# Optimization experiments

Measured on AMD Instinct MI355X. Metric: run time of the kernel, lower is better.

Reference implementation:

```python
import jax, jax.numpy as jnp
import numpy as np

B, P, D, H = 2048, 128, 64, 8
DB = 10  # D_obs + D_pos = 7 + 3, hard-coded in the module


def setup_inputs() -> dict:
    key = jax.random.key(0)
    ks = jax.random.split(key, 10)
    s = lambda fan_in: 1.0 / np.sqrt(fan_in)
    return {
        "x": jax.random.normal(ks[0], (B, D), dtype=jnp.float32),
        "b": jax.random.normal(ks[1], (B, P, DB), dtype=jnp.float32),
        "W_kvx": jax.random.uniform(ks[2], (D, 2 * H * D), jnp.float32, -s(D), s(D)),
        "b_kvx": jax.random.uniform(ks[3], (2 * H * D,), jnp.float32, -s(D), s(D)),
        "W_kvb": jax.random.uniform(ks[4], (DB, 2 * H * D), jnp.float32, -s(DB), s(DB)),
        "b_kvb": jax.random.uniform(ks[5], (2 * H * D,), jnp.float32, -s(DB), s(DB)),
        "W_q": jax.random.uniform(ks[6], (D, H * D), jnp.float32, -s(D), s(D)),
        "b_q": jax.random.uniform(ks[7], (H * D,), jnp.float32, -s(D), s(D)),
        "W_f": jax.random.uniform(ks[8], (H * D, D), jnp.float32, -s(H * D), s(H * D)),
        "b_f": jax.random.uniform(ks[9], (D,), jnp.float32, -s(H * D), s(H * D)),
    }


def reference(x, b, W_kvx, b_kvx, W_kvb, b_kvb, W_q, b_q, W_f, b_f):
    Bn, Dx = x.shape
    _, Pn, _ = b.shape
    # dual projections + broadcast add: [B,1,2HD] + [B,P,2HD]
    kv = (x @ W_kvx + b_kvx)[:, None, :] + (jnp.einsum('bpe,ef->bpf', b, W_kvb) + b_kvb)
    k, v = jnp.split(kv, 2, axis=-1)            # each [B,P,H*D]
    k = k.reshape(Bn, Pn, H, Dx)
    v = v.reshape(Bn, Pn, H, Dx)
    q = (x @ W_q + b_q).reshape(Bn, H, Dx)
    dots = jnp.einsum('bphd,bhd->bph', k, q) / np.sqrt(Dx).astype(np.float32)
    # NOTE: faithful to source — softmax over the HEAD axis (last dim of [B,P,H])
    attn = jax.nn.softmax(dots, axis=-1)
    vals = jnp.einsum('bph,bphd->bhd', attn, v)  # sum over positions P
    out = vals.reshape(Bn, H * Dx) @ W_f + b_f
    return out
```

## Files before the change

### kernel.cpp

```cpp
#include <hip/hip_runtime.h>

#define NB   2048
#define NP   128
#define ND   64
#define NH   8
#define NDB  10
#define HD   512
#define F2   1024
#define XQS  1536

__global__ __launch_bounds__(256) void proj_kernel(
    const float* __restrict__ x, const float* __restrict__ W_kvx,
    const float* __restrict__ b_kvx, const float* __restrict__ W_q,
    const float* __restrict__ b_q, float* __restrict__ XQ)
{
    __shared__ float xs[64][68];
    __shared__ float ws_[64][64];
    const int rt = blockIdx.x;
    const int ct = blockIdx.y;
    const int row0 = rt * 64;
    const int t = threadIdx.x;

    #pragma unroll
    for (int it = 0; it < 16; ++it) {
        int i = t + 256 * it;
        int r = i >> 6, k = i & 63;
        xs[k][r] = x[(row0 + r) * ND + k];
    }
    const float* Wsrc; const float* bsrc; int stride, col0;
    if (ct < 16) { Wsrc = W_kvx; bsrc = b_kvx; stride = F2; col0 = ct * 64; }
    else         { Wsrc = W_q;   bsrc = b_q;   stride = HD; col0 = (ct - 16) * 64; }
    #pragma unroll
    for (int it = 0; it < 16; ++it) {
        int i = t + 256 * it;
        int kr = i >> 6, c = i & 63;
        ws_[kr][c] = Wsrc[kr * stride + col0 + c];
    }
    __syncthreads();

    const int tr = t >> 4, tc = t & 15;
    float acc[4][4] = {};
    for (int k = 0; k < 64; ++k) {
        float4 a = *(const float4*)&xs[k][tr * 4];
        float4 w = *(const float4*)&ws_[k][tc * 4];
        float av[4] = {a.x, a.y, a.z, a.w};
        float wv[4] = {w.x, w.y, w.z, w.w};
        #pragma unroll
        for (int i = 0; i < 4; ++i)
            #pragma unroll
            for (int j = 0; j < 4; ++j)
                acc[i][j] = fmaf(av[i], wv[j], acc[i][j]);
    }
    float4 bias = *(const float4*)&bsrc[col0 + tc * 4];
    const int outcol = ct * 64 + tc * 4;
    #pragma unroll
    for (int i = 0; i < 4; ++i) {
        float4 o;
        o.x = acc[i][0] + bias.x;
        o.y = acc[i][1] + bias.y;
        o.z = acc[i][2] + bias.z;
        o.w = acc[i][3] + bias.w;
        *(float4*)&XQ[(row0 + tr * 4 + i) * XQS + outcol] = o;
    }
}

__global__ __launch_bounds__(256) void attn_kernel(
    const float* __restrict__ bmat, const float* __restrict__ W_kvb,
    const float* __restrict__ b_kvb, const float* __restrict__ XQ,
    float* __restrict__ VALS)
{
    __shared__ float q_s[HD];
    __shared__ float bb_s[NP * NDB];
    __shared__ float dot0[NH];
    __shared__ float Wqkb[NDB][NH];
    __shared__ float partA[4][NH];
    __shared__ float partS[4][NDB][NH];
    __shared__ float A_s[NH];
    __shared__ float S_s[NDB][NH];

    const int b = blockIdx.x;
    const int t = threadIdx.x;
    const int lane = t & 63, w = t >> 6;
    const float* xq = XQ + (size_t)b * XQS;

    q_s[t]       = xq[1024 + t];
    q_s[t + 256] = xq[1024 + t + 256];
    #pragma unroll
    for (int it = 0; it < 5; ++it) {
        int i = t + 256 * it;
        bb_s[i] = bmat[(size_t)b * (NP * NDB) + i];
    }
    __syncthreads();

    #pragma unroll
    for (int iter = 0; iter < 2; ++iter) {
        int f = t + iter * 256;
        float prod = (xq[f] + b_kvb[f]) * q_s[f];
        #pragma unroll
        for (int m = 32; m >= 1; m >>= 1) prod += __shfl_xor(prod, m);
        if (lane == 0) dot0[w + iter * 4] = prod;
    }
    {
        int g = t >> 3, l = t & 7;
        #pragma unroll
        for (int ro = 0; ro < 3; ++ro) {
            int o = g + 32 * ro;
            if (o < 80) {
                int e = o >> 3, hh = o & 7;
                float s = 0.f;
                #pragma unroll
                for (int m = 0; m < 8; ++m) {
                    int d = l + m * 8;
                    s += W_kvb[e * F2 + hh * 64 + d] * q_s[hh * 64 + d];
                }
                #pragma unroll
                for (int mm = 1; mm <= 4; mm <<= 1) s += __shfl_xor(s, mm);
                if (l == 0) Wqkb[e][hh] = s;
            }
        }
    }
    __syncthreads();

    const int h = t & 7;
    const int pbase = t >> 3;
    float aA = 0.f;
    float aS[NDB];
    #pragma unroll
    for (int e = 0; e < NDB; ++e) aS[e] = 0.f;
    #pragma unroll
    for (int it = 0; it < 4; ++it) {
        int p = pbase + it * 32;
        float dot = dot0[h];
        #pragma unroll
        for (int e = 0; e < NDB; ++e) dot += bb_s[p * NDB + e] * Wqkb[e][h];
        dot *= 0.125f;
        float m = dot;
        #pragma unroll
        for (int mm = 1; mm <= 4; mm <<= 1) m = fmaxf(m, __shfl_xor(m, mm));
        float ex = __expf(dot - m);
        float s = ex;
        #pragma unroll
        for (int mm = 1; mm <= 4; mm <<= 1) s += __shfl_xor(s, mm);
        float at = ex / s;
        aA += at;
        #pragma unroll
        for (int e = 0; e < NDB; ++e) aS[e] += at * bb_s[p * NDB + e];
    }
    #pragma unroll
    for (int mm = 8; mm <= 32; mm <<= 1) aA += __shfl_xor(aA, mm);
    #pragma unroll
    for (int e = 0; e < NDB; ++e)
        #pragma unroll
        for (int mm = 8; mm <= 32; mm <<= 1) aS[e] += __shfl_xor(aS[e], mm);
    if (lane < 8) {
        partA[w][lane] = aA;
        #pragma unroll
        for (int e = 0; e < NDB; ++e) partS[w][e][lane] = aS[e];
    }
    __syncthreads();
    if (t < 8)  A_s[t] = partA[0][t] + partA[1][t] + partA[2][t] + partA[3][t];
    if (t < 80) {
        int e = t >> 3, hh = t & 7;
        S_s[e][hh] = partS[0][e][hh] + partS[1][e][hh] + partS[2][e][hh] + partS[3][e][hh];
    }
    __syncthreads();

    #pragma unroll
    for (int iter = 0; iter < 2; ++iter) {
        int f = t + iter * 256;
        int hh = f >> 6;
        float val = A_s[hh] * (xq[512 + f] + b_kvb[512 + f]);
        #pragma unroll
        for (int e = 0; e < NDB; ++e) val += S_s[e][hh] * W_kvb[e * F2 + 512 + f];
        VALS[(size_t)b * HD + f] = val;
    }
}

__global__ __launch_bounds__(256) void out_kernel(
    const float* __restrict__ VALS, const float* __restrict__ W_f,
    const float* __restrict__ b_f, float* __restrict__ out)
{
    __shared__ float vs[HD * 10];
    const int t = threadIdx.x;
    const int row0 = blockIdx.x * 8;
    #pragma unroll
    for (int it = 0; it < 16; ++it) {
        int i = t + 256 * it;
        int r = i >> 9, k = i & 511;
        vs[k * 10 + r] = VALS[(size_t)(row0 + r) * HD + k];
    }
    __syncthreads();
    const int j = t & 63, rg = t >> 6;
    float acc0 = 0.f, acc1 = 0.f;
    for (int k = 0; k < 512; ++k) {
        float wv = W_f[k * 64 + j];
        float2 v = *(const float2*)&vs[k * 10 + rg * 2];
        acc0 = fmaf(v.x, wv, acc0);
        acc1 = fmaf(v.y, wv, acc1);
    }
    float bj = b_f[j];
    out[(size_t)(row0 + rg * 2 + 0) * ND + j] = acc0 + bj;
    out[(size_t)(row0 + rg * 2 + 1) * ND + j] = acc1 + bj;
}

extern "C" void kernel_launch(void* const* d_in, const int* in_sizes, int n_in,
                              void* d_out, int out_size, void* d_ws, size_t ws_size,
                              hipStream_t stream)
{
    const float* x     = (const float*)d_in[0];
    const float* bmat  = (const float*)d_in[1];
    const float* W_kvx = (const float*)d_in[2];
    const float* b_kvx = (const float*)d_in[3];
    const float* W_kvb = (const float*)d_in[4];
    const float* b_kvb = (const float*)d_in[5];
    const float* W_q   = (const float*)d_in[6];
    const float* b_q   = (const float*)d_in[7];
    const float* W_f   = (const float*)d_in[8];
    const float* b_f   = (const float*)d_in[9];
    float* out  = (float*)d_out;
    float* XQ   = (float*)d_ws;
    float* VALS = XQ + (size_t)NB * XQS;

    proj_kernel<<<dim3(32, 24), 256, 0, stream>>>(x, W_kvx, b_kvx, W_q, b_q, XQ);
    attn_kernel<<<NB, 256, 0, stream>>>(bmat, W_kvb, b_kvb, XQ, VALS);
    out_kernel<<<NB / 8, 256, 0, stream>>>(VALS, W_f, b_f, out);
}
```

Measured before the change: 125.0 us.

## Fuse projection, attention and output GEMM into one kernel over 4-row batches

Replaces the three-kernel pipeline (projection GEMM, per-row attention, output GEMM) with a single kernel in which each block handles 4 batch rows. Each wave processes one row's attention, and intermediates stay in shared memory instead of going through the global XQ/VALS workspace. This removes two launches and roughly 16 MB of intermediate global traffic. In exchange, each block re-reads the full W_kvx, W_q and W_f weights from global/L2 with only 4-row reuse, and only 512 blocks are launched.

Measured after the change: 105.5 us. -15.6%, faster.

```diff
diff --git a/kernel.cpp b/kernel.cpp
--- a/kernel.cpp
+++ b/kernel.cpp
@@ -1,206 +1,181 @@
 #include <hip/hip_runtime.h>
 
-#define NB   2048
-#define NP   128
-#define ND   64
-#define NH   8
-#define NDB  10
-#define HD   512
-#define F2   1024
-#define XQS  1536
+#define NDB 10
 
-__global__ __launch_bounds__(256) void proj_kernel(
-    const float* __restrict__ x, const float* __restrict__ W_kvx,
-    const float* __restrict__ b_kvx, const float* __restrict__ W_q,
-    const float* __restrict__ b_q, float* __restrict__ XQ)
+__global__ __launch_bounds__(256) void fused_attn(
+    const float* __restrict__ x, const float* __restrict__ bmat,
+    const float* __restrict__ W_kvx, const float* __restrict__ b_kvx,
+    const float* __restrict__ W_kvb, const float* __restrict__ b_kvb,
+    const float* __restrict__ W_q, const float* __restrict__ b_q,
+    const float* __restrict__ W_f, const float* __restrict__ b_f,
+    float* __restrict__ out)
 {
-    __shared__ float xs[64][68];
-    __shared__ float ws_[64][64];
-    const int rt = blockIdx.x;
-    const int ct = blockIdx.y;
-    const int row0 = rt * 64;
+    __shared__ float x_t[64][4];
+    __shared__ float bb_s[4][1280];
+    __shared__ float xp_s[4][1024];
+    __shared__ float q_s[4][512];
+    __shared__ float dot0_s[4][8];
+    __shared__ float Wqkb_s[4][NDB][8];
+    __shared__ float A_s[4][8];
+    __shared__ float S_s[4][NDB][8];
+    __shared__ float vals_s[512][4];
+    __shared__ float pout[4][4][64];
+
     const int t = threadIdx.x;
+    const int b0 = blockIdx.x * 4;
+    const int lane = t & 63;
+    const int w = t >> 6;
 
-    #pragma unroll
-    for (int it = 0; it < 16; ++it) {
-        int i = t + 256 * it;
-        int r = i >> 6, k = i & 63;
-        xs[k][r] = x[(row0 + r) * ND + k];
-    }
-    const float* Wsrc; const float* bsrc; int stride, col0;
-    if (ct < 16) { Wsrc = W_kvx; bsrc = b_kvx; stride = F2; col0 = ct * 64; }
-    else         { Wsrc = W_q;   bsrc = b_q;   stride = HD; col0 = (ct - 16) * 64; }
-    #pragma unroll
-    for (int it = 0; it < 16; ++it) {
-        int i = t + 256 * it;
-        int kr = i >> 6, c = i & 63;
-        ws_[kr][c] = Wsrc[kr * stride + col0 + c];
+    x_t[t & 63][t >> 6] = x[b0 * 64 + t];
+    {
+        const float4* src = (const float4*)(bmat + (size_t)b0 * 1280);
+        float4* dst = (float4*)bb_s;
+        #pragma unroll
+        for (int it = 0; it < 5; ++it) dst[t + 256 * it] = src[t + 256 * it];
     }
     __syncthreads();
 
-    const int tr = t >> 4, tc = t & 15;
-    float acc[4][4] = {};
-    for (int k = 0; k < 64; ++k) {
-        float4 a = *(const float4*)&xs[k][tr * 4];
-        float4 w = *(const float4*)&ws_[k][tc * 4];
-        float av[4] = {a.x, a.y, a.z, a.w};
-        float wv[4] = {w.x, w.y, w.z, w.w};
+    {
+        float accKV[4][4] = {};
+        float accQ[4][2] = {};
+        const float* pkv = W_kvx + t;
+        const float* pq  = W_q  + t;
+        #pragma unroll 4
+        for (int k = 0; k < 64; ++k) {
+            float4 xv = *(const float4*)&x_t[k][0];
+            float xr[4] = {xv.x, xv.y, xv.z, xv.w};
+            float wkv[4], wq[2];
+            #pragma unroll
+            for (int c = 0; c < 4; ++c) wkv[c] = pkv[k * 1024 + c * 256];
+            #pragma unroll
+            for (int c = 0; c < 2; ++c) wq[c] = pq[k * 512 + c * 256];
+            #pragma unroll
+            for (int r = 0; r < 4; ++r) {
+                #pragma unroll
+                for (int c = 0; c < 4; ++c) accKV[r][c] = fmaf(xr[r], wkv[c], accKV[r][c]);
+                #pragma unroll
+                for (int c = 0; c < 2; ++c) accQ[r][c]  = fmaf(xr[r], wq[c],  accQ[r][c]);
+            }
+        }
         #pragma unroll
-        for (int i = 0; i < 4; ++i)
+        for (int c = 0; c < 4; ++c) {
+            int f = c * 256 + t;
+            float bias = b_kvx[f] + b_kvb[f];
             #pragma unroll
-            for (int j = 0; j < 4; ++j)
-                acc[i][j] = fmaf(av[i], wv[j], acc[i][j]);
+            for (int rr = 0; rr < 4; ++rr) xp_s[rr][f] = accKV[rr][c] + bias;
+        }
+        #pragma unroll
+        for (int c = 0; c < 2; ++c) {
+            int fq = c * 256 + t;
+            float bias = b_q[fq];
+            #pragma unroll
+            for (int rr = 0; rr < 4; ++rr) q_s[rr][fq] = accQ[rr][c] + bias;
+        }
     }
-    float4 bias = *(const float4*)&bsrc[col0 + tc * 4];
-    const int outcol = ct * 64 + tc * 4;
-    #pragma unroll
-    for (int i = 0; i < 4; ++i) {
-        float4 o;
-        o.x = acc[i][0] + bias.x;
-        o.y = acc[i][1] + bias.y;
-        o.z = acc[i][2] + bias.z;
-        o.w = acc[i][3] + bias.w;
-        *(float4*)&XQ[(row0 + tr * 4 + i) * XQS + outcol] = o;
+    __syncthreads();
+
+    const int r = w;
+
+    {
+        int h = lane >> 3, i8 = lane & 7;
+        float s = 0.f;
+        #pragma unroll
+        for (int j = 0; j < 8; ++j) {
+            int d = h * 64 + i8 + j * 8;
+            s = fmaf(xp_s[r][d], q_s[r][d], s);
+        }
+        s += __shfl_xor(s, 1); s += __shfl_xor(s, 2); s += __shfl_xor(s, 4);
+        if (i8 == 0) dot0_s[r][h] = s;
     }
-}
+    {
+        int g = lane >> 3, l = lane & 7;
+        #pragma unroll
+        for (int e = 0; e < NDB; ++e) {
+            float s = 0.f;
+            #pragma unroll
+            for (int m = 0; m < 8; ++m) {
+                int d = g * 64 + l + m * 8;
+                s = fmaf(W_kvb[e * 1024 + d], q_s[r][d], s);
+            }
+            s += __shfl_xor(s, 1); s += __shfl_xor(s, 2); s += __shfl_xor(s, 4);
+            if (l == 0) Wqkb_s[r][e][g] = s;
+        }
+    }
+    __syncthreads();
 
-__global__ __launch_bounds__(256) void attn_kernel(
-    const float* __restrict__ bmat, const float* __restrict__ W_kvb,
-    const float* __restrict__ b_kvb, const float* __restrict__ XQ,
-    float* __restrict__ VALS)
-{
-    __shared__ float q_s[HD];
-    __shared__ float bb_s[NP * NDB];
-    __shared__ float dot0[NH];
-    __shared__ float Wqkb[NDB][NH];
-    __shared__ float partA[4][NH];
-    __shared__ float partS[4][NDB][NH];
-    __shared__ float A_s[NH];
-    __shared__ float S_s[NDB][NH];
-
-    const int b = blockIdx.x;
-    const int t = threadIdx.x;
-    const int lane = t & 63, w = t >> 6;
-    const float* xq = XQ + (size_t)b * XQS;
-
-    q_s[t]       = xq[1024 + t];
-    q_s[t + 256] = xq[1024 + t + 256];
-    #pragma unroll
-    for (int it = 0; it < 5; ++it) {
-        int i = t + 256 * it;
-        bb_s[i] = bmat[(size_t)b * (NP * NDB) + i];
+    {
+        int h = lane & 7, pg = lane >> 3;
+        float aA = 0.f, aS[NDB];
+        #pragma unroll
+        for (int e = 0; e < NDB; ++e) aS[e] = 0.f;
+        #pragma unroll 4
+        for (int it = 0; it < 16; ++it) {
+            int p = pg + 8 * it;
+            float dot = dot0_s[r][h];
+            #pragma unroll
+            for (int e = 0; e < NDB; ++e)
+                dot = fmaf(bb_s[r][p * NDB + e], Wqkb_s[r][e][h], dot);
+            dot *= 0.125f;
+            float m = dot;
+            m = fmaxf(m, __shfl_xor(m, 1));
+            m = fmaxf(m, __shfl_xor(m, 2));
+            m = fmaxf(m, __shfl_xor(m, 4));
+            float ex = __expf(dot - m);
+            float sum = ex;
+            sum += __shfl_xor(sum, 1); sum += __shfl_xor(sum, 2); sum += __shfl_xor(sum, 4);
+            float at = ex * __builtin_amdgcn_rcpf(sum);
+            aA += at;
+            #pragma unroll
+            for (int e = 0; e < NDB; ++e) aS[e] = fmaf(at, bb_s[r][p * NDB + e], aS[e]);
+        }
+        aA += __shfl_xor(aA, 8); aA += __shfl_xor(aA, 16); aA += __shfl_xor(aA, 32);
+        #pragma unroll
+        for (int e = 0; e < NDB; ++e) {
+            aS[e] += __shfl_xor(aS[e], 8);
+            aS[e] += __shfl_xor(aS[e], 16);
+            aS[e] += __shfl_xor(aS[e], 32);
+        }
+        if (pg == 0) {
+            A_s[r][h] = aA;
+            #pragma unroll
+            for (int e = 0; e < NDB; ++e) S_s[r][e][h] = aS[e];
+        }
     }
     __syncthreads();
 
     #pragma unroll
-    for (int iter = 0; iter < 2; ++iter) {
-        int f = t + iter * 256;
-        float prod = (xq[f] + b_kvb[f]) * q_s[f];
+    for (int i = 0; i < 8; ++i) {
+        int f = lane + 64 * i;
+        float v = A_s[r][i] * xp_s[r][512 + f];
         #pragma unroll
-        for (int m = 32; m >= 1; m >>= 1) prod += __shfl_xor(prod, m);
-        if (lane == 0) dot0[w + iter * 4] = prod;
-    }
-    {
-        int g = t >> 3, l = t & 7;
-        #pragma unroll
-        for (int ro = 0; ro < 3; ++ro) {
-            int o = g + 32 * ro;
-            if (o < 80) {
-                int e = o >> 3, hh = o & 7;
-                float s = 0.f;
-                #pragma unroll
-                for (int m = 0; m < 8; ++m) {
-                    int d = l + m * 8;
-                    s += W_kvb[e * F2 + hh * 64 + d] * q_s[hh * 64 + d];
-                }
-                #pragma unroll
-                for (int mm = 1; mm <= 4; mm <<= 1) s += __shfl_xor(s, mm);
-                if (l == 0) Wqkb[e][hh] = s;
-            }
-        }
+        for (int e = 0; e < NDB; ++e)
+            v = fmaf(S_s[r][e][i], W_kvb[e * 1024 + 512 + f], v);
+        vals_s[f][r] = v;
     }
     __syncthreads();
 
-    const int h = t & 7;
-    const int pbase = t >> 3;
-    float aA = 0.f;
-    float aS[NDB];
-    #pragma unroll
-    for (int e = 0; e < NDB; ++e) aS[e] = 0.f;
-    #pragma unroll
-    for (int it = 0; it < 4; ++it) {
-        int p = pbase + it * 32;
-        float dot = dot0[h];
-        #pragma unroll
-        for (int e = 0; e < NDB; ++e) dot += bb_s[p * NDB + e] * Wqkb[e][h];
-        dot *= 0.125f;
-        float m = dot;
-        #pragma unroll
-        for (int mm = 1; mm <= 4; mm <<= 1) m = fmaxf(m, __shfl_xor(m, mm));
-        float ex = __expf(dot - m);
-        float s = ex;
-        #pragma unroll
-        for (int mm = 1; mm <= 4; mm <<= 1) s += __shfl_xor(s, mm);
-        float at = ex / s;
-        aA += at;
-        #pragma unroll
-        for (int e = 0; e < NDB; ++e) aS[e] += at * bb_s[p * NDB + e];
-    }
-    #pragma unroll
-    for (int mm = 8; mm <= 32; mm <<= 1) aA += __shfl_xor(aA, mm);
-    #pragma unroll
-    for (int e = 0; e < NDB; ++e)
-        #pragma unroll
-        for (int mm = 8; mm <= 32; mm <<= 1) aS[e] += __shfl_xor(aS[e], mm);
-    if (lane < 8) {
-        partA[w][lane] = aA;
-        #pragma unroll
-        for (int e = 0; e < NDB; ++e) partS[w][e][lane] = aS[e];
+    {
+        const int j = t & 63, fs = t >> 6;
+        float acc0 = 0.f, acc1 = 0.f, acc2 = 0.f, acc3 = 0.f;
+        #pragma unroll 4
+        for (int fi = 0; fi < 128; ++fi) {
+            int f = fs * 128 + fi;
+            float4 v = *(const float4*)&vals_s[f][0];
+            float wf = W_f[f * 64 + j];
+            acc0 = fmaf(v.x, wf, acc0);
+            acc1 = fmaf(v.y, wf, acc1);
+            acc2 = fmaf(v.z, wf, acc2);
+            acc3 = fmaf(v.w, wf, acc3);
+        }
+        pout[fs][0][j] = acc0; pout[fs][1][j] = acc1;
+        pout[fs][2][j] = acc2; pout[fs][3][j] = acc3;
     }
     __syncthreads();
-    if (t < 8)  A_s[t] = partA[0][t] + partA[1][t] + partA[2][t] + partA[3][t];
-    if (t < 80) {
-        int e = t >> 3, hh = t & 7;
-        S_s[e][hh] = partS[0][e][hh] + partS[1][e][hh] + partS[2][e][hh] + partS[3][e][hh];
+    {
+        const int rr = t >> 6, j = t & 63;
+        float o = pout[0][rr][j] + pout[1][rr][j] + pout[2][rr][j] + pout[3][rr][j] + b_f[j];
+        out[(size_t)(b0 + rr) * 64 + j] = o;
     }
-    __syncthreads();
-
-    #pragma unroll
-    for (int iter = 0; iter < 2; ++iter) {
-        int f = t + iter * 256;
-        int hh = f >> 6;
-        float val = A_s[hh] * (xq[512 + f] + b_kvb[512 + f]);
-        #pragma unroll
-        for (int e = 0; e < NDB; ++e) val += S_s[e][hh] * W_kvb[e * F2 + 512 + f];
-        VALS[(size_t)b * HD + f] = val;
-    }
-}
-
-__global__ __launch_bounds__(256) void out_kernel(
-    const float* __restrict__ VALS, const float* __restrict__ W_f,
-    const float* __restrict__ b_f, float* __restrict__ out)
-{
-    __shared__ float vs[HD * 10];
-    const int t = threadIdx.x;
-    const int row0 = blockIdx.x * 8;
-    #pragma unroll
-    for (int it = 0; it < 16; ++it) {
-        int i = t + 256 * it;
-        int r = i >> 9, k = i & 511;
-        vs[k * 10 + r] = VALS[(size_t)(row0 + r) * HD + k];
-    }
-    __syncthreads();
-    const int j = t & 63, rg = t >> 6;
-    float acc0 = 0.f, acc1 = 0.f;
-    for (int k = 0; k < 512; ++k) {
-        float wv = W_f[k * 64 + j];
-        float2 v = *(const float2*)&vs[k * 10 + rg * 2];
-        acc0 = fmaf(v.x, wv, acc0);
-        acc1 = fmaf(v.y, wv, acc1);
-    }
-    float bj = b_f[j];
-    out[(size_t)(row0 + rg * 2 + 0) * ND + j] = acc0 + bj;
-    out[(size_t)(row0 + rg * 2 + 1) * ND + j] = acc1 + bj;
 }
 
 extern "C" void kernel_launch(void* const* d_in, const int* in_sizes, int n_in,
@@ -217,11 +192,8 @@
     const float* b_q   = (const float*)d_in[7];
     const float* W_f   = (const float*)d_in[8];
     const float* b_f   = (const float*)d_in[9];
-    float* out  = (float*)d_out;
-    float* XQ   = (float*)d_ws;
-    float* VALS = XQ + (size_t)NB * XQS;
+    float* out = (float*)d_out;
 
-    proj_kernel<<<dim3(32, 24), 256, 0, stream>>>(x, W_kvx, b_kvx, W_q, b_q, XQ);
-    attn_kernel<<<NB, 256, 0, stream>>>(bmat, W_kvb, b_kvb, XQ, VALS);
-    out_kernel<<<NB / 8, 256, 0, stream>>>(VALS, W_f, b_f, out);
+    fused_attn<<<512, 256, 0, stream>>>(x, bmat, W_kvx, b_kvx, W_kvb, b_kvb,
+                                        W_q, b_q, W_f, b_f, out);
 }
```
